# Kernel optimization log

Hardware: AMD Instinct MI355X
Metric: run time of the kernel (lower is better)

The kernel has to match this reference:

```python
import jax, jax.numpy as jnp
import numpy as np


def conv1d(x, w, b, pad):
    # x: (B, Cin, T), w: (Cout, Cin, K), b: (Cout,)
    y = jax.lax.conv_general_dilated(x, w, window_strides=(1,), padding=[(pad, pad)],
                                     dimension_numbers=('NCH', 'OIH', 'NCH'))
    return y + b[None, :, None]


def setup_inputs() -> dict:
    key = jax.random.key(0)
    ks = jax.random.split(key, 16)
    B, Cmel, Ctxt, Catt, T1, T2 = 16, 80, 256, 80, 800, 200
    s = 0.05
    return {
        'queries': jax.random.normal(ks[0], (B, Cmel, T1), jnp.float32),
        'keys': jax.random.normal(ks[1], (B, Ctxt, T2), jnp.float32),
        'attn_prior': jax.random.uniform(ks[2], (B, T1, T2), jnp.float32),
        # key_proj: Conv1d(256->512,k=3,pad=1) -> ReLU -> Conv1d(512->80,k=1)
        'kw1': jax.random.normal(ks[3], (Ctxt * 2, Ctxt, 3), jnp.float32) * s,
        'kb1': jax.random.normal(ks[4], (Ctxt * 2,), jnp.float32) * s,
        'kw2': jax.random.normal(ks[5], (Catt, Ctxt * 2, 1), jnp.float32) * s,
        'kb2': jax.random.normal(ks[6], (Catt,), jnp.float32) * s,
        # query_proj (3xconv): 80->160 k3 -> ReLU -> 160->80 k1 -> ReLU -> 80->80 k1
        'qw1': jax.random.normal(ks[7], (Cmel * 2, Cmel, 3), jnp.float32) * s,
        'qb1': jax.random.normal(ks[8], (Cmel * 2,), jnp.float32) * s,
        'qw2': jax.random.normal(ks[9], (Cmel, Cmel * 2, 1), jnp.float32) * s,
        'qb2': jax.random.normal(ks[10], (Cmel,), jnp.float32) * s,
        'qw3': jax.random.normal(ks[11], (Catt, Cmel, 1), jnp.float32) * s,
        'qb3': jax.random.normal(ks[12], (Catt,), jnp.float32) * s,
    }


def reference(queries, keys, attn_prior, kw1, kb1, kw2, kb2, qw1, qb1, qw2, qb2, qw3, qb3):
    # key encoder
    k = jax.nn.relu(conv1d(keys, kw1, kb1, pad=1))
    k = conv1d(k, kw2, kb2, pad=0)                      # (B, Catt, T2)
    # query encoder ('3xconv')
    q = jax.nn.relu(conv1d(queries, qw1, qb1, pad=1))
    q = jax.nn.relu(conv1d(q, qw2, qb2, pad=0))
    q = conv1d(q, qw3, qb3, pad=0)                      # (B, Catt, T1)
    # L2 distance over channels: ||q||^2 + ||k||^2 - 2 q.k (same math as broadcast (q-k)^2 sum)
    q2 = jnp.sum(q * q, axis=1)                         # (B, T1)
    k2 = jnp.sum(k * k, axis=1)                         # (B, T2)
    qk = jnp.einsum('bct,bcs->bts', q, k)               # (B, T1, T2)
    attn = -0.0005 * (q2[:, :, None] + k2[:, None, :] - 2.0 * qk)[:, None]  # (B,1,T1,T2)
    attn = jax.nn.log_softmax(attn, axis=3) + jnp.log(attn_prior[:, None] + 1e-8)
    return attn
```

## Files before the change

### kernel.cpp

```cpp
#include <hip/hip_runtime.h>
#include <cstdint>
#include <cmath>

using short8  = __attribute__((ext_vector_type(8))) short;
using short4v = __attribute__((ext_vector_type(4))) short;
using floatx4 = __attribute__((ext_vector_type(4))) float;

__device__ __forceinline__ short f2bf(float f) {
  union { float f; unsigned u; } x; x.f = f;
  unsigned r = x.u + 0x7FFFu + ((x.u >> 16) & 1u);
  return (short)(r >> 16);
}

__device__ __forceinline__ void gl_lds16(const short* g, short* l) {
  __builtin_amdgcn_global_load_lds(
      (const __attribute__((address_space(1))) void*)g,
      (__attribute__((address_space(3))) void*)l, 16, 0, 0);
}

__global__ __launch_bounds__(256) void prep_kernel(
    const float* __restrict__ keys, const float* __restrict__ queries,
    const float* __restrict__ kw1, const float* __restrict__ kw2,
    const float* __restrict__ qw1, const float* __restrict__ qw2,
    const float* __restrict__ qw3,
    short* __restrict__ kT0, short* __restrict__ qT0,
    short* __restrict__ w1, short* __restrict__ w2, short* __restrict__ w3,
    short* __restrict__ w4, short* __restrict__ w5)
{
  const int bid = blockIdx.x, tid = threadIdx.x;
  __shared__ float xs[32][65];

  if (bid < 1136) {
    const float* src; short* dst; int CIN, T, CP, bx, by, b;
    if (bid < 512) {
      src = keys; dst = kT0; CIN = 256; T = 200; CP = 256;
      bx = bid & 3; by = (bid >> 2) & 7; b = bid >> 5;
    } else {
      int b2 = bid - 512;
      src = queries; dst = qT0; CIN = 80; T = 800; CP = 96;
      bx = b2 % 13; by = (b2 / 13) % 3; b = b2 / 39;
    }
    const int t0 = bx * 64, ci0 = by * 32;
    for (int i = tid; i < 32 * 64; i += 256) {
      int row = i >> 6, col = i & 63;
      float v = 0.f;
      if (ci0 + row < CIN && t0 + col < T)
        v = src[((size_t)b * CIN + ci0 + row) * T + t0 + col];
      xs[row][col] = v;
    }
    __syncthreads();
    int t = tid >> 2, c8 = (tid & 3) * 8;
    if (t0 + t < T) {
      short8 o;
      #pragma unroll
      for (int j = 0; j < 8; ++j) o[j] = f2bf(xs[c8 + j][t]);
      *(short8*)&dst[((size_t)b * T + t0 + t) * CP + ci0 + c8] = o;
    }
  } else {
    int blk = bid - 1136;
    const float* src; short* dst; int base;
    int CoP, CiP, Cout, CIN, K; bool isW1 = false;
    if      (blk < 384) { src=kw1; dst=w1; base=0;   CoP=512; CiP=256; Cout=512; CIN=256; K=3; isW1=true; }
    else if (blk < 432) { src=kw2; dst=w2; base=384; CoP=96;  CiP=512; Cout=80;  CIN=512; K=1; }
    else if (blk < 486) { src=qw1; dst=w3; base=432; CoP=192; CiP=96;  Cout=160; CIN=80;  K=3; }
    else if (blk < 504) { src=qw2; dst=w4; base=486; CoP=96;  CiP=192; Cout=80;  CIN=160; K=1; }
    else                { src=qw3; dst=w5; base=504; CoP=96;  CiP=96;  Cout=80;  CIN=80;  K=1; }
    int tot = K * CoP * CiP;
    int b0 = (blk - base) * 1024;
    for (int e = 0; e < 4; ++e) {
      int gi = b0 + e * 256 + tid;
      if (gi < tot) {
        int dk  = gi / (CoP * CiP);
        int rem = gi - dk * (CoP * CiP);
        int co  = rem / CiP, ci = rem - (rem / CiP) * CiP;
        float v = (co < Cout && ci < CIN) ? src[((size_t)co * CIN + ci) * K + dk] : 0.f;
        int idx = gi;
        if (isW1) idx = (((ci >> 5) * 3 + dk) * 512 + co) * 32 + (ci & 31);
        dst[idx] = f2bf(v);
      }
    }
  }
}

__global__ __launch_bounds__(256) void conv_k3_kernel(
    const short* __restrict__ kT0, const short* __restrict__ qT0,
    const short* __restrict__ w1, const short* __restrict__ w3,
    const short* __restrict__ w4, const short* __restrict__ w5,
    const float* __restrict__ kb1, const float* __restrict__ qb1,
    const float* __restrict__ qb2, const float* __restrict__ qb3,
    short* __restrict__ kT1, short* __restrict__ qF)
{
  __shared__ __align__(16) short smem[29904];
  const int tid = threadIdx.x, wid = tid >> 6, lane = tid & 63;
  const int q = lane >> 4, m = lane & 15;

  if (blockIdx.x < 512) {
    const int blk = blockIdx.x;
    const int b = blk >> 5, co0 = ((blk >> 2) & 7) * 64, t0 = (blk & 3) * 64;
    const int wy = wid >> 1, wx = wid & 1;
    short* xs = smem;
    short* asb0 = smem + 17424;
    short* asb1 = smem + 23568;

    floatx4 acc[2][2];
    #pragma unroll
    for (int i = 0; i < 2; ++i)
      #pragma unroll
      for (int j = 0; j < 2; ++j) acc[i][j] = (floatx4){0.f, 0.f, 0.f, 0.f};

    for (int i = tid; i < 66 * 32; i += 256) {
      int row = i >> 5, c8 = (i & 31) * 8;
      int t = t0 + row - 1;
      int4 v = {0, 0, 0, 0};
      if (t >= 0 && t < 200)
        v = *(const int4*)&kT0[((size_t)b * 200 + t) * 256 + c8];
      *(int4*)&xs[row * 264 + c8] = v;
    }
    {
      const int wv = tid >> 6;
      #pragma unroll
      for (int c = 0; c < 3; ++c) {
        const short* g = w1 + ((size_t)(0 * 3 + c) * 512 + co0) * 32 + tid * 8;
        short* l = asb0 + c * 2048 + wv * 512;
        gl_lds16(g, l);
      }
    }
    __syncthreads();

    int cur = 0;
    for (int c0 = 0; c0 < 8; ++c0) {
      short* as_cur = cur ? asb1 : asb0;
      if (c0 < 7) {
        short* asn = cur ? asb0 : asb1;
        const int wv = tid >> 6;
        #pragma unroll
        for (int c = 0; c < 3; ++c) {
          const short* g = w1 + ((size_t)((c0 + 1) * 3 + c) * 512 + co0) * 32 + tid * 8;
          gl_lds16(g, asn + c * 2048 + wv * 512);
        }
      }
      #pragma unroll
      for (int dk = 0; dk < 3; ++dk) {
        short8 fa0 = *(const short8*)&as_cur[dk * 2048 + (wy * 32 + m) * 32 + q * 8];
        short8 fa1 = *(const short8*)&as_cur[dk * 2048 + (wy * 32 + 16 + m) * 32 + q * 8];
        #pragma unroll
        for (int j = 0; j < 2; ++j) {
          short8 fb = *(const short8*)&xs[(wx * 32 + j * 16 + m + dk) * 264 + c0 * 32 + q * 8];
          acc[0][j] = __builtin_amdgcn_mfma_f32_16x16x32_bf16(fa0, fb, acc[0][j], 0, 0, 0);
          acc[1][j] = __builtin_amdgcn_mfma_f32_16x16x32_bf16(fa1, fb, acc[1][j], 0, 0, 0);
        }
      }
      __syncthreads();
      cur ^= 1;
    }
    #pragma unroll
    for (int i = 0; i < 2; ++i) {
      #pragma unroll
      for (int j = 0; j < 2; ++j) {
        #pragma unroll
        for (int r = 0; r < 4; ++r) {
          int co = co0 + wy * 32 + i * 16 + q * 4 + r;
          int t  = t0 + wx * 32 + j * 16 + m;
          if (t < 200) {
            float v = fmaxf(acc[i][j][r] + kb1[co], 0.f);
            kT1[((size_t)b * 200 + t) * 512 + co] = f2bf(v);
          }
        }
      }
    }
  } else {
    const int qbid = blockIdx.x - 512;
    const int b = qbid / 13, t0 = (qbid % 13) * 64;
    short* xs2 = smem;
    short* y1c = smem + 6864;
    short* y2c = smem + 22224;

    floatx4 accq[3][4];
    #pragma unroll
    for (int f = 0; f < 3; ++f)
      #pragma unroll
      for (int tf = 0; tf < 4; ++tf) accq[f][tf] = (floatx4){0.f, 0.f, 0.f, 0.f};

    for (int i = tid; i < 66 * 12; i += 256) {
      int row = i / 12, g = i - (i / 12) * 12;
      int t = t0 + row - 1;
      int4 v = {0, 0, 0, 0};
      if (t >= 0 && t < 800)
        v = *(const int4*)&qT0[((size_t)b * 800 + t) * 96 + g * 8];
      *(int4*)&xs2[row * 104 + g * 8] = v;
    }
    __syncthreads();

    for (int c0 = 0; c0 < 3; ++c0) {
      #pragma unroll
      for (int dk = 0; dk < 3; ++dk) {
        short8 fa[3];
        #pragma unroll
        for (int f = 0; f < 3; ++f)
          fa[f] = *(const short8*)&w3[((size_t)(dk * 192 + wid * 48 + f * 16 + m)) * 96
                                      + c0 * 32 + q * 8];
        #pragma unroll
        for (int tf = 0; tf < 4; ++tf) {
          short8 fb = *(const short8*)&xs2[(tf * 16 + m + dk) * 104 + c0 * 32 + q * 8];
          #pragma unroll
          for (int f = 0; f < 3; ++f)
            accq[f][tf] = __builtin_amdgcn_mfma_f32_16x16x32_bf16(fa[f], fb, accq[f][tf], 0, 0, 0);
        }
      }
    }
    __syncthreads();
    #pragma unroll
    for (int f = 0; f < 3; ++f) {
      #pragma unroll
      for (int tf = 0; tf < 4; ++tf) {
        int co = wid * 48 + f * 16 + q * 4;
        int t  = tf * 16 + m;
        short4v o;
        #pragma unroll
        for (int r = 0; r < 4; ++r) {
          float bv = (co + r < 160) ? qb1[co + r] : 0.f;
          o[r] = f2bf(fmaxf(accq[f][tf][r] + bv, 0.f));
        }
        *(short4v*)&y1c[(co >> 5) * 2560 + t * 40 + (co & 31)] = o;
      }
    }
    __syncthreads();

    floatx4 acc2q[6];
    #pragma unroll
    for (int f = 0; f < 6; ++f) acc2q[f] = (floatx4){0.f, 0.f, 0.f, 0.f};
    #pragma unroll
    for (int c = 0; c < 6; ++c) {
      short8 fb = *(const short8*)&y1c[c * 2560 + (wid * 16 + m) * 40 + q * 8];
      #pragma unroll
      for (int f = 0; f < 6; ++f) {
        short8 fa = *(const short8*)&w4[((size_t)(f * 16 + m)) * 192 + c * 32 + q * 8];
        acc2q[f] = __builtin_amdgcn_mfma_f32_16x16x32_bf16(fa, fb, acc2q[f], 0, 0, 0);
      }
    }
    #pragma unroll
    for (int f = 0; f < 6; ++f) {
      int co = f * 16 + q * 4;
      int t  = wid * 16 + m;
      short4v o;
      #pragma unroll
      for (int r = 0; r < 4; ++r) {
        float bv = (co + r < 80) ? qb2[co + r] : 0.f;
        o[r] = f2bf(fmaxf(acc2q[f][r] + bv, 0.f));
      }
      *(short4v*)&y2c[(co >> 5) * 2560 + t * 40 + (co & 31)] = o;
    }
    __syncthreads();

    floatx4 acc3q[6];
    #pragma unroll
    for (int f = 0; f < 6; ++f) acc3q[f] = (floatx4){0.f, 0.f, 0.f, 0.f};
    #pragma unroll
    for (int c = 0; c < 3; ++c) {
      short8 fb = *(const short8*)&y2c[c * 2560 + (wid * 16 + m) * 40 + q * 8];
      #pragma unroll
      for (int f = 0; f < 6; ++f) {
        short8 fa = *(const short8*)&w5[((size_t)(f * 16 + m)) * 96 + c * 32 + q * 8];
        acc3q[f] = __builtin_amdgcn_mfma_f32_16x16x32_bf16(fa, fb, acc3q[f], 0, 0, 0);
      }
    }
    int t = t0 + wid * 16 + m;
    if (t < 800) {
      #pragma unroll
      for (int f = 0; f < 6; ++f) {
        int co = f * 16 + q * 4;
        short4v o;
        #pragma unroll
        for (int r = 0; r < 4; ++r) {
          float bv = (co + r < 80) ? qb3[co + r] : 0.f;
          o[r] = f2bf(acc3q[f][r] + bv);
        }
        *(short4v*)&qF[((size_t)b * 800 + t) * 96 + co] = o;
      }
    }
  }
}

__global__ __launch_bounds__(64) void kconv2_kernel(
    const short* __restrict__ kT1, const short* __restrict__ w2,
    const float* __restrict__ kb2, short* __restrict__ kF)
{
  const int blk = blockIdx.x;
  const int b = blk / 13, t0 = (blk - b * 13) * 16;
  const int lane = threadIdx.x & 63;
  const int q = lane >> 4, m = lane & 15;
  const int t = t0 + m;
  const bool tv = (t < 200);

  floatx4 acc[6];
  #pragma unroll
  for (int f = 0; f < 6; ++f) acc[f] = (floatx4){0.f, 0.f, 0.f, 0.f};

  #pragma unroll
  for (int c = 0; c < 16; ++c) {
    short8 fb;
    if (tv) fb = *(const short8*)&kT1[((size_t)b * 200 + t) * 512 + c * 32 + q * 8];
    else    fb = (short8){0,0,0,0,0,0,0,0};
    #pragma unroll
    for (int f = 0; f < 6; ++f) {
      short8 fa = *(const short8*)&w2[((size_t)(f * 16 + m)) * 512 + c * 32 + q * 8];
      acc[f] = __builtin_amdgcn_mfma_f32_16x16x32_bf16(fa, fb, acc[f], 0, 0, 0);
    }
  }
  if (tv) {
    #pragma unroll
    for (int f = 0; f < 6; ++f) {
      int co = f * 16 + q * 4;
      short4v o;
      #pragma unroll
      for (int r = 0; r < 4; ++r) {
        float bv = (co + r < 80) ? kb2[co + r] : 0.f;
        o[r] = f2bf(acc[f][r] + bv);
      }
      *(short4v*)&kF[((size_t)b * 200 + t) * 96 + co] = o;
    }
  }
}

__global__ __launch_bounds__(256) void attn_mfma(
    const short* __restrict__ qT, const short* __restrict__ kT,
    const float* __restrict__ prior, float* __restrict__ out)
{
  const int b = blockIdx.y, t1_0 = blockIdx.x * 64;
  const int tid = threadIdx.x, wid = tid >> 6, lane = tid & 63;
  const int q = lane >> 4, m = lane & 15;

  __shared__ __align__(16) char smem[51200];
  short* aq = (short*)smem;
  short* bk = (short*)(smem + 13312);
  float* k2s = (float*)(smem + 29952);
  float* sstage = (float*)smem;

  floatx4 acc[13];
  #pragma unroll
  for (int f = 0; f < 13; ++f) acc[f] = (floatx4){0.f, 0.f, 0.f, 0.f};

  for (int i = tid; i < 64 * 12; i += 256) {
    int row = i / 12, g = i - (i / 12) * 12;
    int4 v = {0, 0, 0, 0};
    if (t1_0 + row < 800)
      v = *(const int4*)&qT[((size_t)b * 800 + t1_0 + row) * 96 + g * 8];
    *(int4*)&aq[row * 104 + g * 8] = v;
  }

  float k2acc = 0.f;
  for (int c = 0; c < 3; ++c) {
    __syncthreads();
    for (int i = tid; i < 208 * 4; i += 256) {
      int row = i >> 2, g = i & 3;
      int4 v = {0, 0, 0, 0};
      if (row < 200)
        v = *(const int4*)&kT[((size_t)b * 200 + row) * 96 + c * 32 + g * 8];
      *(int4*)&bk[row * 40 + g * 8] = v;
    }
    __syncthreads();
    if (tid < 208) {
      #pragma unroll
      for (int g = 0; g < 4; ++g) {
        short8 s = *(const short8*)&bk[tid * 40 + g * 8];
        #pragma unroll
        for (int j = 0; j < 8; ++j) {
          union { unsigned u; float f; } x; x.u = ((unsigned)(unsigned short)s[j]) << 16;
          k2acc = fmaf(x.f, x.f, k2acc);
        }
      }
    }
    short8 fa = *(const short8*)&aq[(wid * 16 + m) * 104 + c * 32 + q * 8];
    #pragma unroll
    for (int f = 0; f < 13; ++f) {
      short8 fb = *(const short8*)&bk[(f * 16 + m) * 40 + q * 8];
      acc[f] = __builtin_amdgcn_mfma_f32_16x16x32_bf16(fa, fb, acc[f], 0, 0, 0);
    }
  }
  if (tid < 208) k2s[tid] = k2acc;
  __syncthreads();

  float k2v[13];
  #pragma unroll
  for (int f = 0; f < 13; ++f) k2v[f] = k2s[f * 16 + m];

  float mx[4] = {-INFINITY, -INFINITY, -INFINITY, -INFINITY};
  #pragma unroll
  for (int f = 0; f < 13; ++f) {
    bool valid = (f * 16 + m) < 200;
    #pragma unroll
    for (int r = 0; r < 4; ++r) {
      float v = valid ? (0.001f * acc[f][r] - 0.0005f * k2v[f]) : -INFINITY;
      acc[f][r] = v;
      mx[r] = fmaxf(mx[r], v);
    }
  }
  #pragma unroll
  for (int msk = 1; msk < 16; msk <<= 1)
    #pragma unroll
    for (int r = 0; r < 4; ++r) mx[r] = fmaxf(mx[r], __shfl_xor(mx[r], msk));
  float sm[4] = {0.f, 0.f, 0.f, 0.f};
  #pragma unroll
  for (int f = 0; f < 13; ++f)
    #pragma unroll
    for (int r = 0; r < 4; ++r) sm[r] += __expf(acc[f][r] - mx[r]);
  #pragma unroll
  for (int msk = 1; msk < 16; msk <<= 1)
    #pragma unroll
    for (int r = 0; r < 4; ++r) sm[r] += __shfl_xor(sm[r], msk);
  float lse[4];
  #pragma unroll
  for (int r = 0; r < 4; ++r) lse[r] = mx[r] + __logf(sm[r]);

  __syncthreads();
  #pragma unroll
  for (int f = 0; f < 13; ++f) {
    int col = f * 16 + m;
    if (col < 200) {
      #pragma unroll
      for (int r = 0; r < 4; ++r)
        sstage[(wid * 16 + q * 4 + r) * 200 + col] = acc[f][r] - lse[r];
    }
  }
  __syncthreads();

  for (int i = tid; i < 64 * 50; i += 256) {
    int row = i / 50, seg = i - (i / 50) * 50;
    int t1 = t1_0 + row;
    if (t1 < 800) {
      size_t o = ((size_t)b * 800 + t1) * 200 + seg * 4;
      floatx4 pv = *(const floatx4*)&prior[o];
      floatx4 sv = *(const floatx4*)&sstage[row * 200 + seg * 4];
      floatx4 ov;
      #pragma unroll
      for (int j = 0; j < 4; ++j) ov[j] = sv[j] + __logf(pv[j] + 1e-8f);
      *(floatx4*)&out[o] = ov;
    }
  }
}

extern "C" void kernel_launch(void* const* d_in, const int* in_sizes, int n_in,
                              void* d_out, int out_size, void* d_ws, size_t ws_size,
                              hipStream_t stream) {
  const float* queries = (const float*)d_in[0];
  const float* keys    = (const float*)d_in[1];
  const float* prior   = (const float*)d_in[2];
  const float* kw1 = (const float*)d_in[3];
  const float* kb1 = (const float*)d_in[4];
  const float* kw2 = (const float*)d_in[5];
  const float* kb2 = (const float*)d_in[6];
  const float* qw1 = (const float*)d_in[7];
  const float* qb1 = (const float*)d_in[8];
  const float* qw2 = (const float*)d_in[9];
  const float* qb2 = (const float*)d_in[10];
  const float* qw3 = (const float*)d_in[11];
  const float* qb3 = (const float*)d_in[12];
  float* out = (float*)d_out;

  short* p = (short*)d_ws;
  short* kT0 = p;  p += (size_t)3200 * 256;
  short* qT0 = p;  p += (size_t)12800 * 96;
  short* w1  = p;  p += (size_t)3 * 512 * 256;
  short* w2  = p;  p += (size_t)96 * 512;
  short* w3  = p;  p += (size_t)3 * 192 * 96;
  short* w4  = p;  p += (size_t)96 * 192;
  short* w5  = p;  p += (size_t)96 * 96;
  short* kT1 = p;  p += (size_t)3200 * 512;
  short* kF  = p;  p += (size_t)3200 * 96;
  short* qF  = p;  p += (size_t)12800 * 96;

  prep_kernel<<<dim3(1649), 256, 0, stream>>>(keys, queries, kw1, kw2, qw1, qw2, qw3,
                                              kT0, qT0, w1, w2, w3, w4, w5);
  conv_k3_kernel<<<dim3(720), 256, 0, stream>>>(kT0, qT0, w1, w3, w4, w5,
                                                kb1, qb1, qb2, qb3, kT1, qF);
  kconv2_kernel<<<dim3(208), 64, 0, stream>>>(kT1, w2, kb2, kF);
  attn_mfma<<<dim3(13, 16), 256, 0, stream>>>(qF, kF, prior, out);
}
```

Before: 146.8 us.

## Stream key-conv input per channel chunk with double buffering to shrink LDS

The key k=3 conv branch used to stage the whole 66x256 input tile in LDS up front. It now loads only the 32-channel slice needed per iteration, prefetching it into registers alongside the weight prefetch and storing it into a double-buffered small tile after the MFMAs. The query branch buffers are re-laid out so y2c aliases the input region, cutting total shared memory from about 58KB to 45KB. This is meant to overlap input loads with compute and raise occupancy, at the cost of extra per-iteration global loads and register pressure.

```diff
diff --git a/kernel.cpp b/kernel.cpp
--- a/kernel.cpp
+++ b/kernel.cpp
@@ -90,17 +90,15 @@
     const float* __restrict__ qb2, const float* __restrict__ qb3,
     short* __restrict__ kT1, short* __restrict__ qF)
 {
-  __shared__ __align__(16) short smem[29904];
+  __shared__ __align__(16) short smem[23040];
   const int tid = threadIdx.x, wid = tid >> 6, lane = tid & 63;
   const int q = lane >> 4, m = lane & 15;
 
   if (blockIdx.x < 512) {
     const int blk = blockIdx.x;
-    const int b = blk >> 5, co0 = ((blk >> 2) & 7) * 64, t0 = (blk & 3) * 64;
+    const int bb = blk >> 5, co0 = ((blk >> 2) & 7) * 64, t0 = (blk & 3) * 64;
     const int wy = wid >> 1, wx = wid & 1;
-    short* xs = smem;
-    short* asb0 = smem + 17424;
-    short* asb1 = smem + 23568;
+    const int wv = tid >> 6;
 
     floatx4 acc[2][2];
     #pragma unroll
@@ -108,49 +106,60 @@
       #pragma unroll
       for (int j = 0; j < 2; ++j) acc[i][j] = (floatx4){0.f, 0.f, 0.f, 0.f};
 
-    for (int i = tid; i < 66 * 32; i += 256) {
-      int row = i >> 5, c8 = (i & 31) * 8;
-      int t = t0 + row - 1;
-      int4 v = {0, 0, 0, 0};
-      if (t >= 0 && t < 200)
-        v = *(const int4*)&kT0[((size_t)b * 200 + t) * 256 + c8];
-      *(int4*)&xs[row * 264 + c8] = v;
-    }
-    {
-      const int wv = tid >> 6;
+    auto xload = [&](int c0s, int4& a, int4& bvv) {
+      { int row = tid >> 2, g = tid & 3;
+        int t = t0 + row - 1;
+        a = (int4){0,0,0,0};
+        if (t >= 0 && t < 200)
+          a = *(const int4*)&kT0[((size_t)bb * 200 + t) * 256 + c0s * 32 + g * 8]; }
+      bvv = (int4){0,0,0,0};
+      if (tid < 8) {
+        int i1 = tid + 256, row = i1 >> 2, g = i1 & 3;
+        int t = t0 + row - 1;
+        if (t >= 0 && t < 200)
+          bvv = *(const int4*)&kT0[((size_t)bb * 200 + t) * 256 + c0s * 32 + g * 8];
+      }
+    };
+    auto xstore = [&](const int4& a, const int4& bvv, int xoff) {
+      { int row = tid >> 2, g = tid & 3; *(int4*)&smem[xoff + row * 40 + g * 8] = a; }
+      if (tid < 8) { int i1 = tid + 256, row = i1 >> 2, g = i1 & 3;
+        *(int4*)&smem[xoff + row * 40 + g * 8] = bvv; }
+    };
+    auto wissue = [&](int c0s, int aoff) {
       #pragma unroll
       for (int c = 0; c < 3; ++c) {
-        const short* g = w1 + ((size_t)(0 * 3 + c) * 512 + co0) * 32 + tid * 8;
-        short* l = asb0 + c * 2048 + wv * 512;
-        gl_lds16(g, l);
-      }
-    }
+        const short* g = w1 + ((size_t)(c0s * 3 + c) * 512 + co0) * 32 + tid * 8;
+        gl_lds16(g, &smem[aoff + c * 2048 + wv * 512]);
+      }
+    };
+
+    { int4 a, bvv; xload(0, a, bvv); wissue(0, 5280); xstore(a, bvv, 0); }
     __syncthreads();
 
     int cur = 0;
     for (int c0 = 0; c0 < 8; ++c0) {
-      short* as_cur = cur ? asb1 : asb0;
+      const int xo = cur ? 2640 : 0;
+      const int ao = cur ? 11424 : 5280;
+      int4 xa, xb;
       if (c0 < 7) {
-        short* asn = cur ? asb0 : asb1;
-        const int wv = tid >> 6;
-        #pragma unroll
-        for (int c = 0; c < 3; ++c) {
-          const short* g = w1 + ((size_t)((c0 + 1) * 3 + c) * 512 + co0) * 32 + tid * 8;
-          gl_lds16(g, asn + c * 2048 + wv * 512);
-        }
+        wissue(c0 + 1, cur ? 5280 : 11424);
+        xload(c0 + 1, xa, xb);
       }
       #pragma unroll
       for (int dk = 0; dk < 3; ++dk) {
-        short8 fa0 = *(const short8*)&as_cur[dk * 2048 + (wy * 32 + m) * 32 + q * 8];
-        short8 fa1 = *(const short8*)&as_cur[dk * 2048 + (wy * 32 + 16 + m) * 32 + q * 8];
+        short8 fa0 = *(const short8*)&smem[ao + dk * 2048 + (wy * 32 + m) * 32 + q * 8];
+        short8 fa1 = *(const short8*)&smem[ao + dk * 2048 + (wy * 32 + 16 + m) * 32 + q * 8];
         #pragma unroll
         for (int j = 0; j < 2; ++j) {
-          short8 fb = *(const short8*)&xs[(wx * 32 + j * 16 + m + dk) * 264 + c0 * 32 + q * 8];
+          short8 fb = *(const short8*)&smem[xo + (wx * 32 + j * 16 + m + dk) * 40 + q * 8];
           acc[0][j] = __builtin_amdgcn_mfma_f32_16x16x32_bf16(fa0, fb, acc[0][j], 0, 0, 0);
           acc[1][j] = __builtin_amdgcn_mfma_f32_16x16x32_bf16(fa1, fb, acc[1][j], 0, 0, 0);
         }
       }
-      __syncthreads();
+      if (c0 < 7) {
+        xstore(xa, xb, cur ? 0 : 2640);
+        __syncthreads();
+      }
       cur ^= 1;
     }
     #pragma unroll
@@ -163,7 +172,7 @@
           int t  = t0 + wx * 32 + j * 16 + m;
           if (t < 200) {
             float v = fmaxf(acc[i][j][r] + kb1[co], 0.f);
-            kT1[((size_t)b * 200 + t) * 512 + co] = f2bf(v);
+            kT1[((size_t)bb * 200 + t) * 512 + co] = f2bf(v);
           }
         }
       }
@@ -172,8 +181,8 @@
     const int qbid = blockIdx.x - 512;
     const int b = qbid / 13, t0 = (qbid % 13) * 64;
     short* xs2 = smem;
-    short* y1c = smem + 6864;
-    short* y2c = smem + 22224;
+    short* y1c = smem + 7680;
+    short* y2c = smem;
 
     floatx4 accq[3][4];
     #pragma unroll
```

Result: faster. 140.0 us (-4.6%).
